# Performance work log

Hardware: AMD Instinct MI355X
Metric: run time of the kernel (lower is better)

## Reference

```python
import jax, jax.numpy as jnp
import numpy as np

K = 8
DIM = 64
NUM_BLOCKS = 12
BN_EPS = 1e-5
LRELU_SLOPE = 0.01  # torch nn.LeakyReLU default negative_slope


def knn_indices(xyz, k):
    # xyz: [b, 3, n] -> idx [b, n, k] of k nearest neighbors (self included)
    x = jnp.transpose(xyz, (0, 2, 1))  # [b, n, 3]
    sq = jnp.sum(x * x, axis=-1)  # [b, n]
    d2 = sq[:, :, None] - 2.0 * jnp.einsum('bnd,bmd->bnm', x, x) + sq[:, None, :]
    _, idx = jax.lax.top_k(-d2, k)  # k smallest distances
    return idx


def group_point(points, idx):
    # points [b, d, n], idx [b, n, k] -> grouped [b, d, k, n]
    g = jax.vmap(lambda p, i: p[:, i])(points, idx)  # [b, d, n, k]
    return jnp.transpose(g, (0, 1, 3, 2))


def setup_inputs() -> dict:
    key = jax.random.key(0)
    ks = jax.random.split(key, 6)
    b, n = 8, 4096
    xyz = jax.random.normal(ks[0], (b, 3, n), dtype=jnp.float32)
    points = jax.random.normal(ks[1], (b, DIM, n), dtype=jnp.float32)
    # per-block params (note: the module's second Conv2d per block is never used
    # in forward — layers[4*idx+2] is applied to both center and grouped points)
    conv_w = jax.random.normal(ks[2], (NUM_BLOCKS, DIM, DIM), dtype=jnp.float32) * (1.0 / np.sqrt(DIM))
    conv_b = jax.random.normal(ks[3], (NUM_BLOCKS, DIM), dtype=jnp.float32) * 0.01
    bn_gamma = 1.0 + 0.1 * jax.random.normal(ks[4], (NUM_BLOCKS, DIM), dtype=jnp.float32)
    bn_beta = 0.1 * jax.random.normal(ks[5], (NUM_BLOCKS, DIM), dtype=jnp.float32)
    return {"xyz": xyz, "points": points, "conv_w": conv_w, "conv_b": conv_b,
            "bn_gamma": bn_gamma, "bn_beta": bn_beta}


def reference(xyz, points, conv_w, conv_b, bn_gamma, bn_beta):
    idx = knn_indices(xyz, K)  # fixed graph, computed once in block 0

    def block(p, params):
        w, b, g, be = params  # [DIM,DIM], [DIM], [DIM], [DIM]
        shortcut = p
        # BatchNorm1d (training-mode batch stats over batch & point dims)
        mean = jnp.mean(p, axis=(0, 2), keepdims=True)
        var = jnp.var(p, axis=(0, 2), keepdims=True)
        h = (p - mean) * jax.lax.rsqrt(var + BN_EPS) * g[None, :, None] + be[None, :, None]
        # LeakyReLU
        h = jnp.where(h >= 0, h, LRELU_SLOPE * h)
        # gather neighbor features: [b, d, k, n]
        grouped = group_point(h, idx)
        # shared 1x1 conv on center and grouped points
        center = jnp.einsum('od,bdn->bon', w, h) + b[None, :, None]            # [b,d,n]
        gconv = jnp.einsum('od,bdkn->bokn', w, grouped) + b[None, :, None, None]  # [b,d,k,n]
        # mean over concat([center[:, :, None], gconv], axis=2) == (center + sum_k gconv) / (k+1)
        new_p = (center + jnp.sum(gconv, axis=2)) / (K + 1) + shortcut
        return new_p, None

    out, _ = jax.lax.scan(block, points, (conv_w, conv_b, bn_gamma, bn_beta))
    return out
```

## Files before the change

kernel.cpp:

```cpp
#include <hip/hip_runtime.h>
#include <hip/hip_bf16.h>

#define NB     8
#define NPTS   4096
#define DIMC   64
#define KNN_K  8
#define NBLK   12
#define NREP   8

__global__ __launch_bounds__(256) void prep_kernel(
        const float* __restrict__ xyz, float4* __restrict__ pts4g,
        float* __restrict__ stats) {
#pragma clang fp contract(off)
    int g = blockIdx.x * 256 + threadIdx.x;
    if (g < 13 * NREP * 128) stats[g] = 0.0f;
    int b = g >> 12, j = g & 4095;
    const float* xb = xyz + (size_t)b * 3 * NPTS;
    float x = xb[j];
    float y = xb[NPTS + j];
    float z = xb[2 * NPTS + j];
    float sq = (x * x + y * y) + z * z;
    pts4g[g] = make_float4(x, y, z, sq);
}

__global__ __launch_bounds__(256) void cast_kernel(
        const float* __restrict__ pts,
        float* __restrict__ P0, float* __restrict__ stats0) {
    __shared__ __align__(16) float tr[64 * 65];
    __shared__ float slotA[4 * 64], slotB[4 * 64];
    int wg = blockIdx.x;
    int b = wg & 7;
    int n0 = (wg >> 3) << 6;
    int rep = (wg >> 3) & (NREP - 1);
    int tid = threadIdx.x;
    int lane6 = tid & 63;
    int grp = tid >> 6;

    #pragma unroll
    for (int k = 0; k < 16; ++k) {
        int d = grp + (k << 2);
        float v = pts[(((size_t)((b << 6) + d)) << 12) + n0 + lane6];
        tr[d * 65 + lane6] = v;
    }
    __syncthreads();
    int c = lane6;
    float s = 0.0f, s2 = 0.0f;
    #pragma unroll
    for (int k = 0; k < 16; ++k) {
        int p = grp + (k << 2);
        float v = tr[c * 65 + p];
        P0[((size_t)((b << 12) + n0 + p)) * 64 + c] = v;
        s += v; s2 += v * v;
    }
    slotA[grp * 64 + c] = s;
    slotB[grp * 64 + c] = s2;
    __syncthreads();
    if (tid < 64) {
        float t = slotA[tid] + slotA[64 + tid] + slotA[128 + tid] + slotA[192 + tid];
        atomicAdd(&stats0[rep * 128 + tid], t);
    } else if (tid < 128) {
        int cc = tid - 64;
        float t = slotB[cc] + slotB[64 + cc] + slotB[128 + cc] + slotB[192 + cc];
        atomicAdd(&stats0[rep * 128 + 64 + cc], t);
    }
}

#define INS(KEY) do { \
    double key = (KEY); \
    double n0 = fmin(k0, key); \
    double n1 = fmin(k1, fmax(k0, key)); \
    double n2 = fmin(k2, fmax(k1, key)); \
    double n3 = fmin(k3, fmax(k2, key)); \
    double n4 = fmin(k4, fmax(k3, key)); \
    double n5 = fmin(k5, fmax(k4, key)); \
    double n6 = fmin(k6, fmax(k5, key)); \
    double n7 = fmin(k7, fmax(k6, key)); \
    k0 = n0; k1 = n1; k2 = n2; k3 = n3; \
    k4 = n4; k5 = n5; k6 = n6; k7 = n7; } while (0)

__global__ __launch_bounds__(512) void knn_kernel(
        const float4* __restrict__ pts4g, int* __restrict__ idx) {
#pragma clang fp contract(off)
    __shared__ double stash[4 * 9 * 128];
    int wg = blockIdx.x;
    int b = wg >> 5;
    int q0 = (wg & 31) << 7;
    int tid = threadIdx.x;

    int lane  = tid & 63;
    int wave  = tid >> 6;
    int chunk = wave & 3;
    int qgrp  = wave >> 2;
    int q_l   = (qgrp << 6) | lane;

    const float4* cb = pts4g + ((size_t)b << 12);
    float4 qp = cb[q0 + q_l];

    double k0, k1, k2, k3, k4, k5, k6, k7;
    k0 = k1 = k2 = k3 = k4 = k5 = k6 = k7 = __builtin_inf();
    float bd7f = 3.4e38f;

    int chu = __builtin_amdgcn_readfirstlane(chunk);
    const float4* cc = cb + ((size_t)chu << 10);
    int jg0 = chu << 10;

    for (int jo = 0; jo < 128; jo += 8) {
        float d2v[8];
        #pragma unroll
        for (int u = 0; u < 8; ++u) {
            float4 p = cc[jo + u];
            float dot = (qp.x * p.x + qp.y * p.y) + qp.z * p.z;
            d2v[u] = (qp.w - 2.0f * dot) + p.w;
        }
        #pragma unroll
        for (int u = 0; u < 8; ++u) {
            unsigned long long kb =
                __double_as_longlong((double)d2v[u]) |
                (unsigned long long)(jg0 + jo + u);
            INS(__longlong_as_double(kb));
        }
    }
    bd7f = (float)k7;

    for (int jo = 128; jo < 1024; jo += 8) {
        float d2v[8];
        unsigned hm = 0u;
        #pragma unroll
        for (int u = 0; u < 8; ++u) {
            float4 p = cc[jo + u];
            float dot = (qp.x * p.x + qp.y * p.y) + qp.z * p.z;
            float d2 = (qp.w - 2.0f * dot) + p.w;
            d2v[u] = d2;
            hm |= (d2 < bd7f) ? (1u << u) : 0u;
        }
        while (__any(hm != 0u)) {
            if (hm) {
                int u = __builtin_ctz(hm);
                hm &= hm - 1u;
                float t0 = (u & 1) ? d2v[1] : d2v[0];
                float t1 = (u & 1) ? d2v[3] : d2v[2];
                float t2 = (u & 1) ? d2v[5] : d2v[4];
                float t3 = (u & 1) ? d2v[7] : d2v[6];
                float s0 = (u & 2) ? t1 : t0;
                float s1 = (u & 2) ? t3 : t2;
                float d2 = (u & 4) ? s1 : s0;
                unsigned long long kb =
                    __double_as_longlong((double)d2) |
                    (unsigned long long)(jg0 + jo + u);
                INS(__longlong_as_double(kb));
            }
        }
        bd7f = (float)k7;
    }

    {
        double* S = &stash[(chunk * 9) * 128 + q_l];
        S[0 * 128] = k0; S[1 * 128] = k1; S[2 * 128] = k2; S[3 * 128] = k3;
        S[4 * 128] = k4; S[5 * 128] = k5; S[6 * 128] = k6; S[7 * 128] = k7;
        S[8 * 128] = __builtin_inf();
    }
    __syncthreads();

    if (tid < 128) {
        int h0 = 0, h1 = 0, h2 = 0, h3 = 0;
        int* op = idx + ((size_t)(b * NPTS + q0 + tid)) * 8;
        #pragma unroll
        for (int t = 0; t < 8; ++t) {
            double b0 = stash[(0 * 9 + h0) * 128 + tid];
            double b1 = stash[(1 * 9 + h1) * 128 + tid];
            double b2 = stash[(2 * 9 + h2) * 128 + tid];
            double b3 = stash[(3 * 9 + h3) * 128 + tid];
            double best = b0; int bc = 0;
            if (b1 < best) { best = b1; bc = 1; }
            if (b2 < best) { best = b2; bc = 2; }
            if (b3 < best) { best = b3; bc = 3; }
            h0 += (bc == 0); h1 += (bc == 1);
            h2 += (bc == 2); h3 += (bc == 3);
            op[t] = (int)(__double_as_longlong(best) & 0xFFFULL);
        }
    }
}

__global__ __launch_bounds__(256) void block_kernel(
        const float* __restrict__ Pin, float* __restrict__ Pout,
        const float* __restrict__ statsIn, float* __restrict__ statsOut,
        const float* __restrict__ Wp, const float* __restrict__ Bp,
        const float* __restrict__ Gp, const float* __restrict__ Betap,
        const int* __restrict__ gidx, float* __restrict__ dout, int last) {
    __shared__ __align__(16) float Wt[64 * 68];
    __shared__ __align__(16) float mt[64 * 68];
    __shared__ __align__(16) float selft[64 * 64];
    __shared__ __align__(16) int   idxl[64 * 8];
    __shared__ __align__(16) float scale_l[64], shift_l[64], bias_l[64];
    __shared__ float slot[4 * 128];

    int wg = blockIdx.x;
    int b = wg & 7;
    int n0 = (wg >> 3) << 6;
    int rep = (wg >> 3) & (NREP - 1);
    int tid = threadIdx.x;

    const float* Pb = Pin + (((size_t)b) << 18);

    if (tid < 128) {
        ((int4*)idxl)[tid] = ((const int4*)(gidx + ((size_t)(b * NPTS + n0)) * 8))[tid];
    }
    #pragma unroll
    for (int k = 0; k < 4; ++k) {
        int lin = tid + (k << 8);
        ((float4*)selft)[lin] = ((const float4*)&Pb[(size_t)n0 << 6])[lin];
    }
    #pragma unroll
    for (int k = 0; k < 16; ++k) {
        int lin = tid + (k << 8);
        int o = lin >> 6, d = lin & 63;
        Wt[d * 68 + o] = Wp[lin];
    }
    if (tid < 64) {
        int c = tid;
        float sum = 0.0f, sumsq = 0.0f;
        #pragma unroll
        for (int r = 0; r < NREP; ++r) {
            sum   += statsIn[r * 128 + c];
            sumsq += statsIn[r * 128 + 64 + c];
        }
        float mean = sum * (1.0f / 32768.0f);
        float var  = sumsq * (1.0f / 32768.0f) - mean * mean;
        float rs   = 1.0f / sqrtf(var + 1e-5f);
        float sc   = Gp[c] * rs;
        scale_l[c] = sc;
        shift_l[c] = Betap[c] - mean * sc;
        bias_l[c]  = Bp[c];
    }
    __syncthreads();

    {
        int cq = tid & 15;
        int pg = tid >> 4;
        int c4 = cq << 2;
        float4 sc4 = *(const float4*)&scale_l[c4];
        float4 sh4 = *(const float4*)&shift_l[c4];
        float4 r[4];
        #pragma unroll
        for (int i = 0; i < 4; ++i) {
            int pt = (pg << 2) + i;
            int4 ja = *(const int4*)&idxl[pt * 8];
            int4 jb = *(const int4*)&idxl[pt * 8 + 4];
            float4 v[9];
            v[0] = *(const float4*)&selft[(pt << 6) + c4];
            v[1] = *(const float4*)&Pb[(((size_t)ja.x) << 6) + c4];
            v[2] = *(const float4*)&Pb[(((size_t)ja.y) << 6) + c4];
            v[3] = *(const float4*)&Pb[(((size_t)ja.z) << 6) + c4];
            v[4] = *(const float4*)&Pb[(((size_t)ja.w) << 6) + c4];
            v[5] = *(const float4*)&Pb[(((size_t)jb.x) << 6) + c4];
            v[6] = *(const float4*)&Pb[(((size_t)jb.y) << 6) + c4];
            v[7] = *(const float4*)&Pb[(((size_t)jb.z) << 6) + c4];
            v[8] = *(const float4*)&Pb[(((size_t)jb.w) << 6) + c4];
            float4 a = make_float4(0.f, 0.f, 0.f, 0.f);
            #pragma unroll
            for (int k = 0; k < 9; ++k) {
                float hx = v[k].x * sc4.x + sh4.x;
                float hy = v[k].y * sc4.y + sh4.y;
                float hz = v[k].z * sc4.z + sh4.z;
                float hw = v[k].w * sc4.w + sh4.w;
                a.x += fmaxf(hx, 0.01f * hx);
                a.y += fmaxf(hy, 0.01f * hy);
                a.z += fmaxf(hz, 0.01f * hz);
                a.w += fmaxf(hw, 0.01f * hw);
            }
            r[i] = make_float4(a.x * (1.0f / 9.0f), a.y * (1.0f / 9.0f),
                               a.z * (1.0f / 9.0f), a.w * (1.0f / 9.0f));
        }
        int pb4 = pg << 2;
        *(float4*)&mt[(c4 + 0) * 68 + pb4] = make_float4(r[0].x, r[1].x, r[2].x, r[3].x);
        *(float4*)&mt[(c4 + 1) * 68 + pb4] = make_float4(r[0].y, r[1].y, r[2].y, r[3].y);
        *(float4*)&mt[(c4 + 2) * 68 + pb4] = make_float4(r[0].z, r[1].z, r[2].z, r[3].z);
        *(float4*)&mt[(c4 + 3) * 68 + pb4] = make_float4(r[0].w, r[1].w, r[2].w, r[3].w);
    }
    __syncthreads();

    int o0 = (tid & 15) << 2;
    int p0 = (tid >> 4) << 2;
    float4 acc[4];
    {
        float4 bias4 = *(const float4*)&bias_l[o0];
        acc[0] = bias4; acc[1] = bias4; acc[2] = bias4; acc[3] = bias4;
    }
    #pragma unroll
    for (int d = 0; d < 64; ++d) {
        float4 wv = *(const float4*)&Wt[d * 68 + o0];
        float4 a  = *(const float4*)&mt[d * 68 + p0];
        acc[0].x += wv.x * a.x; acc[0].y += wv.y * a.x; acc[0].z += wv.z * a.x; acc[0].w += wv.w * a.x;
        acc[1].x += wv.x * a.y; acc[1].y += wv.y * a.y; acc[1].z += wv.z * a.y; acc[1].w += wv.w * a.y;
        acc[2].x += wv.x * a.z; acc[2].y += wv.y * a.z; acc[2].z += wv.z * a.z; acc[2].w += wv.w * a.z;
        acc[3].x += wv.x * a.w; acc[3].y += wv.y * a.w; acc[3].z += wv.z * a.w; acc[3].w += wv.w * a.w;
    }

    #pragma unroll
    for (int j = 0; j < 4; ++j) {
        float4 r = *(const float4*)&selft[((p0 + j) << 6) + o0];
        acc[j].x += r.x; acc[j].y += r.y; acc[j].z += r.z; acc[j].w += r.w;
    }

    if (!last) {
        float* PbOut = Pout + ((((size_t)b) << 12) + n0) * 64;
        #pragma unroll
        for (int j = 0; j < 4; ++j)
            *(float4*)&PbOut[((size_t)(p0 + j)) * 64 + o0] = acc[j];

        float4 s, s2;
        s.x = acc[0].x + acc[1].x + acc[2].x + acc[3].x;
        s.y = acc[0].y + acc[1].y + acc[2].y + acc[3].y;
        s.z = acc[0].z + acc[1].z + acc[2].z + acc[3].z;
        s.w = acc[0].w + acc[1].w + acc[2].w + acc[3].w;
        s2.x = acc[0].x*acc[0].x + acc[1].x*acc[1].x + acc[2].x*acc[2].x + acc[3].x*acc[3].x;
        s2.y = acc[0].y*acc[0].y + acc[1].y*acc[1].y + acc[2].y*acc[2].y + acc[3].y*acc[3].y;
        s2.z = acc[0].z*acc[0].z + acc[1].z*acc[1].z + acc[2].z*acc[2].z + acc[3].z*acc[3].z;
        s2.w = acc[0].w*acc[0].w + acc[1].w*acc[1].w + acc[2].w*acc[2].w + acc[3].w*acc[3].w;
        #pragma unroll
        for (int m = 16; m <= 32; m <<= 1) {
            s.x += __shfl_xor(s.x, m, 64);  s.y += __shfl_xor(s.y, m, 64);
            s.z += __shfl_xor(s.z, m, 64);  s.w += __shfl_xor(s.w, m, 64);
            s2.x += __shfl_xor(s2.x, m, 64); s2.y += __shfl_xor(s2.y, m, 64);
            s2.z += __shfl_xor(s2.z, m, 64); s2.w += __shfl_xor(s2.w, m, 64);
        }
        if ((tid & 63) < 16) {
            int w = tid >> 6;
            slot[w * 128 + o0 + 0] = s.x;  slot[w * 128 + o0 + 1] = s.y;
            slot[w * 128 + o0 + 2] = s.z;  slot[w * 128 + o0 + 3] = s.w;
            slot[w * 128 + 64 + o0 + 0] = s2.x; slot[w * 128 + 64 + o0 + 1] = s2.y;
            slot[w * 128 + 64 + o0 + 2] = s2.z; slot[w * 128 + 64 + o0 + 3] = s2.w;
        }
        __syncthreads();
        if (tid < 128) {
            float t = slot[tid] + slot[128 + tid] + slot[256 + tid] + slot[384 + tid];
            atomicAdd(&statsOut[rep * 128 + tid], t);
        }
    } else {
        __syncthreads();
        float* stage = mt;
        #pragma unroll
        for (int j = 0; j < 4; ++j) {
            stage[(o0 + 0) * 64 + p0 + j] = acc[j].x;
            stage[(o0 + 1) * 64 + p0 + j] = acc[j].y;
            stage[(o0 + 2) * 64 + p0 + j] = acc[j].z;
            stage[(o0 + 3) * 64 + p0 + j] = acc[j].w;
        }
        __syncthreads();
        #pragma unroll
        for (int k = 0; k < 16; ++k) {
            int lin = tid + (k << 8);
            int o = lin >> 6, pt = lin & 63;
            dout[(((size_t)((b << 6) + o)) << 12) + n0 + pt] = stage[lin];
        }
    }
}

extern "C" void kernel_launch(void* const* d_in, const int* in_sizes, int n_in,
                              void* d_out, int out_size, void* d_ws, size_t ws_size,
                              hipStream_t stream) {
    const float* xyz    = (const float*)d_in[0];
    const float* pts    = (const float*)d_in[1];
    const float* conv_w = (const float*)d_in[2];
    const float* conv_b = (const float*)d_in[3];
    const float* gamma  = (const float*)d_in[4];
    const float* beta   = (const float*)d_in[5];
    float* out = (float*)d_out;

    char* ws = (char*)d_ws;
    float*  P0    = (float*)(ws);
    float*  P1    = (float*)(ws + (size_t)8 * 1024 * 1024);
    int*    idx   = (int*)  (ws + (size_t)16 * 1024 * 1024);
    float*  stats = (float*)(ws + (size_t)17 * 1024 * 1024);
    float4* pts4g = (float4*)(ws + (size_t)18 * 1024 * 1024);

    prep_kernel<<<128, 256, 0, stream>>>(xyz, pts4g, stats);
    cast_kernel<<<512, 256, 0, stream>>>(pts, P0, stats);
    knn_kernel<<<256, 512, 0, stream>>>(pts4g, idx);

    float* Pbuf[2] = {P0, P1};
    for (int t = 0; t < NBLK; ++t) {
        block_kernel<<<512, 256, 0, stream>>>(
            Pbuf[t & 1], Pbuf[(t + 1) & 1],
            stats + (size_t)t * NREP * 128, stats + (size_t)(t + 1) * NREP * 128,
            conv_w + (size_t)t * 4096, conv_b + (size_t)t * 64,
            gamma + (size_t)t * 64, beta + (size_t)t * 64,
            idx, out, (t == NBLK - 1) ? 1 : 0);
    }
}
```

Baseline: 309.1 us.

## Replace FP32 FMA conv GEMM with split-bf16 MFMA (3-term) in block kernel

Each block's 64x64 conv on the aggregated features now runs on matrix cores. Weights and activations are split into high and low bf16 planes, and three bf16 MFMA products (hh, hl, lh) approximate FP32 accuracy. The shared-memory layout changes to bf16 planes with padded rows, and the epilogue and stats reduction are remapped to the MFMA output layout. The GEMM is a small share of a kernel dominated by gathers. The split adds conversion work, and output stores become scalar rather than float4.

```diff
diff --git a/kernel.cpp b/kernel.cpp
--- a/kernel.cpp
+++ b/kernel.cpp
@@ -7,6 +7,17 @@
 #define KNN_K  8
 #define NBLK   12
 #define NREP   8
+
+typedef __attribute__((ext_vector_type(8))) short short8;
+typedef __attribute__((ext_vector_type(4))) float f32x4;
+
+__device__ __forceinline__ void bsplit(float v, unsigned short& h, unsigned short& l) {
+    unsigned b = __float_as_uint(v);
+    h = (unsigned short)(b >> 16);
+    float hf = __uint_as_float(b & 0xFFFF0000u);
+    float lf = v - hf;
+    l = (unsigned short)(__float_as_uint(lf) >> 16);
+}
 
 __global__ __launch_bounds__(256) void prep_kernel(
         const float* __restrict__ xyz, float4* __restrict__ pts4g,
@@ -181,14 +192,18 @@
     }
 }
 
+#define AH_OFF 0
+#define AL_OFF (64 * 72)
+#define WH_OFF (2 * 64 * 72)
+#define WL_OFF (3 * 64 * 72)
+
 __global__ __launch_bounds__(256) void block_kernel(
         const float* __restrict__ Pin, float* __restrict__ Pout,
         const float* __restrict__ statsIn, float* __restrict__ statsOut,
         const float* __restrict__ Wp, const float* __restrict__ Bp,
         const float* __restrict__ Gp, const float* __restrict__ Betap,
         const int* __restrict__ gidx, float* __restrict__ dout, int last) {
-    __shared__ __align__(16) float Wt[64 * 68];
-    __shared__ __align__(16) float mt[64 * 68];
+    __shared__ __align__(16) unsigned short planes[4 * 64 * 72];
     __shared__ __align__(16) float selft[64 * 64];
     __shared__ __align__(16) int   idxl[64 * 8];
     __shared__ __align__(16) float scale_l[64], shift_l[64], bias_l[64];
@@ -211,10 +226,15 @@
         ((float4*)selft)[lin] = ((const float4*)&Pb[(size_t)n0 << 6])[lin];
     }
     #pragma unroll
-    for (int k = 0; k < 16; ++k) {
+    for (int k = 0; k < 4; ++k) {
         int lin = tid + (k << 8);
-        int o = lin >> 6, d = lin & 63;
-        Wt[d * 68 + o] = Wp[lin];
+        float4 wv = ((const float4*)Wp)[lin];
+        int o = lin >> 4, d4 = (lin & 15) << 2;
+        unsigned short hx, hy, hz, hw, lx, ly, lz, lw;
+        bsplit(wv.x, hx, lx); bsplit(wv.y, hy, ly);
+        bsplit(wv.z, hz, lz); bsplit(wv.w, hw, lw);
+        *(ushort4*)&planes[WH_OFF + o * 72 + d4] = make_ushort4(hx, hy, hz, hw);
+        *(ushort4*)&planes[WL_OFF + o * 72 + d4] = make_ushort4(lx, ly, lz, lw);
     }
     if (tid < 64) {
         int c = tid;
@@ -240,7 +260,6 @@
         int c4 = cq << 2;
         float4 sc4 = *(const float4*)&scale_l[c4];
         float4 sh4 = *(const float4*)&shift_l[c4];
-        float4 r[4];
         #pragma unroll
         for (int i = 0; i < 4; ++i) {
             int pt = (pg << 2) + i;
@@ -268,68 +287,98 @@
                 a.z += fmaxf(hz, 0.01f * hz);
                 a.w += fmaxf(hw, 0.01f * hw);
             }
-            r[i] = make_float4(a.x * (1.0f / 9.0f), a.y * (1.0f / 9.0f),
-                               a.z * (1.0f / 9.0f), a.w * (1.0f / 9.0f));
-        }
-        int pb4 = pg << 2;
-        *(float4*)&mt[(c4 + 0) * 68 + pb4] = make_float4(r[0].x, r[1].x, r[2].x, r[3].x);
-        *(float4*)&mt[(c4 + 1) * 68 + pb4] = make_float4(r[0].y, r[1].y, r[2].y, r[3].y);
-        *(float4*)&mt[(c4 + 2) * 68 + pb4] = make_float4(r[0].z, r[1].z, r[2].z, r[3].z);
-        *(float4*)&mt[(c4 + 3) * 68 + pb4] = make_float4(r[0].w, r[1].w, r[2].w, r[3].w);
+            float mx = a.x * (1.0f / 9.0f), my = a.y * (1.0f / 9.0f);
+            float mz = a.z * (1.0f / 9.0f), mw = a.w * (1.0f / 9.0f);
+            unsigned short hx2, hy2, hz2, hw2, lx2, ly2, lz2, lw2;
+            bsplit(mx, hx2, lx2); bsplit(my, hy2, ly2);
+            bsplit(mz, hz2, lz2); bsplit(mw, hw2, lw2);
+            *(ushort4*)&planes[AH_OFF + pt * 72 + c4] = make_ushort4(hx2, hy2, hz2, hw2);
+            *(ushort4*)&planes[AL_OFF + pt * 72 + c4] = make_ushort4(lx2, ly2, lz2, lw2);
+        }
     }
     __syncthreads();
 
-    int o0 = (tid & 15) << 2;
-    int p0 = (tid >> 4) << 2;
-    float4 acc[4];
-    {
-        float4 bias4 = *(const float4*)&bias_l[o0];
-        acc[0] = bias4; acc[1] = bias4; acc[2] = bias4; acc[3] = bias4;
-    }
-    #pragma unroll
-    for (int d = 0; d < 64; ++d) {
-        float4 wv = *(const float4*)&Wt[d * 68 + o0];
-        float4 a  = *(const float4*)&mt[d * 68 + p0];
-        acc[0].x += wv.x * a.x; acc[0].y += wv.y * a.x; acc[0].z += wv.z * a.x; acc[0].w += wv.w * a.x;
-        acc[1].x += wv.x * a.y; acc[1].y += wv.y * a.y; acc[1].z += wv.z * a.y; acc[1].w += wv.w * a.y;
-        acc[2].x += wv.x * a.z; acc[2].y += wv.y * a.z; acc[2].z += wv.z * a.z; acc[2].w += wv.w * a.z;
-        acc[3].x += wv.x * a.w; acc[3].y += wv.y * a.w; acc[3].z += wv.z * a.w; acc[3].w += wv.w * a.w;
-    }
-
-    #pragma unroll
-    for (int j = 0; j < 4; ++j) {
-        float4 r = *(const float4*)&selft[((p0 + j) << 6) + o0];
-        acc[j].x += r.x; acc[j].y += r.y; acc[j].z += r.z; acc[j].w += r.w;
+    int lane = tid & 63;
+    int w    = tid >> 6;
+    int g    = lane >> 4;
+    int c    = lane & 15;
+    int ptb  = w << 4;
+
+    short8 a_h[2], a_l[2];
+    #pragma unroll
+    for (int s = 0; s < 2; ++s) {
+        int off = (ptb + c) * 72 + (s << 5) + (g << 3);
+        a_h[s] = *(const short8*)&planes[AH_OFF + off];
+        a_l[s] = *(const short8*)&planes[AL_OFF + off];
+    }
+
+    f32x4 out[4];
+    #pragma unroll
+    for (int ot = 0; ot < 4; ++ot) {
+        int co = (ot << 4) + c;
+        short8 b_h[2], b_l[2];
+        #pragma unroll
+        for (int s = 0; s < 2; ++s) {
+            int off = co * 72 + (s << 5) + (g << 3);
+            b_h[s] = *(const short8*)&planes[WH_OFF + off];
+            b_l[s] = *(const short8*)&planes[WL_OFF + off];
+        }
+        f32x4 acc = {0.f, 0.f, 0.f, 0.f};
+        acc = __builtin_amdgcn_mfma_f32_16x16x32_bf16(a_h[0], b_h[0], acc, 0, 0, 0);
+        acc = __builtin_amdgcn_mfma_f32_16x16x32_bf16(a_h[1], b_h[1], acc, 0, 0, 0);
+        acc = __builtin_amdgcn_mfma_f32_16x16x32_bf16(a_h[0], b_l[0], acc, 0, 0, 0);
+        acc = __builtin_amdgcn_mfma_f32_16x16x32_bf16(a_h[1], b_l[1], acc, 0, 0, 0);
+        acc = __builtin_amdgcn_mfma_f32_16x16x32_bf16(a_l[0], b_h[0], acc, 0, 0, 0);
+        acc = __builtin_amdgcn_mfma_f32_16x16x32_bf16(a_l[1], b_h[1], acc, 0, 0, 0);
+        out[ot] = acc;
+    }
+
+    #pragma unroll
+    for (int ot = 0; ot < 4; ++ot) {
+        int co = (ot << 4) + c;
+        float bv = bias_l[co];
+        #pragma unroll
+        for (int j = 0; j < 4; ++j) {
+            int pt = ptb + (g << 2) + j;
+            out[ot][j] += bv + selft[(pt << 6) + co];
+        }
     }
 
     if (!last) {
         float* PbOut = Pout + ((((size_t)b) << 12) + n0) * 64;
         #pragma unroll
-        for (int j = 0; j < 4; ++j)
-            *(float4*)&PbOut[((size_t)(p0 + j)) * 64 + o0] = acc[j];
-
-        float4 s, s2;
-        s.x = acc[0].x + acc[1].x + acc[2].x + acc[3].x;
-        s.y = acc[0].y + acc[1].y + acc[2].y + acc[3].y;
-        s.z = acc[0].z + acc[1].z + acc[2].z + acc[3].z;
-        s.w = acc[0].w + acc[1].w + acc[2].w + acc[3].w;
-        s2.x = acc[0].x*acc[0].x + acc[1].x*acc[1].x + acc[2].x*acc[2].x + acc[3].x*acc[3].x;
-        s2.y = acc[0].y*acc[0].y + acc[1].y*acc[1].y + acc[2].y*acc[2].y + acc[3].y*acc[3].y;
-        s2.z = acc[0].z*acc[0].z + acc[1].z*acc[1].z + acc[2].z*acc[2].z + acc[3].z*acc[3].z;
-        s2.w = acc[0].w*acc[0].w + acc[1].w*acc[1].w + acc[2].w*acc[2].w + acc[3].w*acc[3].w;
+        for (int j = 0; j < 4; ++j) {
+            int pt = ptb + (g << 2) + j;
+            #pragma unroll
+            for (int ot = 0; ot < 4; ++ot)
+                PbOut[(size_t)pt * 64 + (ot << 4) + c] = out[ot][j];
+        }
+
+        float sv[4], qv[4];
+        #pragma unroll
+        for (int ot = 0; ot < 4; ++ot) {
+            float s = 0.f, q = 0.f;
+            #pragma unroll
+            for (int j = 0; j < 4; ++j) {
+                float v = out[ot][j];
+                s += v; q += v * v;
+            }
+            sv[ot] = s; qv[ot] = q;
+        }
         #pragma unroll
         for (int m = 16; m <= 32; m <<= 1) {
-            s.x += __shfl_xor(s.x, m, 64);  s.y += __shfl_xor(s.y, m, 64);
-            s.z += __shfl_xor(s.z, m, 64);  s.w += __shfl_xor(s.w, m, 64);
-            s2.x += __shfl_xor(s2.x, m, 64); s2.y += __shfl_xor(s2.y, m, 64);
-            s2.z += __shfl_xor(s2.z, m, 64); s2.w += __shfl_xor(s2.w, m, 64);
-        }
-        if ((tid & 63) < 16) {
-            int w = tid >> 6;
-            slot[w * 128 + o0 + 0] = s.x;  slot[w * 128 + o0 + 1] = s.y;
-            slot[w * 128 + o0 + 2] = s.z;  slot[w * 128 + o0 + 3] = s.w;
-            slot[w * 128 + 64 + o0 + 0] = s2.x; slot[w * 128 + 64 + o0 + 1] = s2.y;
-            slot[w * 128 + 64 + o0 + 2] = s2.z; slot[w * 128 + 64 + o0 + 3] = s2.w;
+            #pragma unroll
+            for (int ot = 0; ot < 4; ++ot) {
+                sv[ot] += __shfl_xor(sv[ot], m, 64);
+                qv[ot] += __shfl_xor(qv[ot], m, 64);
+            }
+        }
+        if (lane < 16) {
+            #pragma unroll
+            for (int ot = 0; ot < 4; ++ot) {
+                slot[w * 128 + (ot << 4) + lane]      = sv[ot];
+                slot[w * 128 + 64 + (ot << 4) + lane] = qv[ot];
+            }
         }
         __syncthreads();
         if (tid < 128) {
@@ -338,20 +387,20 @@
         }
     } else {
         __syncthreads();
-        float* stage = mt;
-        #pragma unroll
-        for (int j = 0; j < 4; ++j) {
-            stage[(o0 + 0) * 64 + p0 + j] = acc[j].x;
-            stage[(o0 + 1) * 64 + p0 + j] = acc[j].y;
-            stage[(o0 + 2) * 64 + p0 + j] = acc[j].z;
-            stage[(o0 + 3) * 64 + p0 + j] = acc[j].w;
+        float* stage = (float*)planes;
+        #pragma unroll
+        for (int ot = 0; ot < 4; ++ot) {
+            int co = (ot << 4) + c;
+            #pragma unroll
+            for (int j = 0; j < 4; ++j)
+                stage[co * 65 + ptb + (g << 2) + j] = out[ot][j];
         }
         __syncthreads();
         #pragma unroll
         for (int k = 0; k < 16; ++k) {
             int lin = tid + (k << 8);
             int o = lin >> 6, pt = lin & 63;
-            dout[(((size_t)((b << 6) + o)) << 12) + n0 + pt] = stage[lin];
+            dout[(((size_t)((b << 6) + o)) << 12) + n0 + pt] = stage[o * 65 + pt];
         }
     }
 }
```

Result: faster. 284.9 us, median of 3 (-7.8%).
